# Optimization experiments

Hardware: AMD Instinct MI355X
Metric: run time of the kernel (lower is better)

Reference implementation:

```python
import jax, jax.numpy as jnp
import numpy as np

BASIS_SIZE = 256          # levels of the bitfield code
R_MAX = 1.0               # quantization range for normalized weights
QMAX = BASIS_SIZE // 2 - 1  # 127 -> symmetric int8-style grid
EPS = 1e-8


def setup_inputs() -> dict:
    key = jax.random.key(0)
    kx, kw, kb = jax.random.split(key, 3)
    B, S, D_IN, D_OUT = 4, 2048, 4096, 4096
    x = jax.random.normal(kx, (B, S, D_IN), dtype=jnp.float32)
    W = jax.random.normal(kw, (D_OUT, D_IN), dtype=jnp.float32)
    bias = jax.random.normal(kb, (D_OUT,), dtype=jnp.float32)
    return {"x": x, "W": W, "bias": bias}


def _bitfield_dequant_weight(W):
    # per-output-row L2 norm (p=2, dim=1 in torch)
    weight_norms = jnp.sqrt(jnp.sum(W * W, axis=1))          # [out]
    W_normalized = W / (weight_norms[:, None] + EPS)          # rows ~unit norm
    # bitfield encode/decode: uniform symmetric quantization to BASIS_SIZE
    # levels in [-R_MAX, R_MAX]
    scale = R_MAX / QMAX
    Wq = jnp.round(jnp.clip(W_normalized, -R_MAX, R_MAX) / scale) * scale
    return Wq, weight_norms


def reference(x, W, bias):
    Wq, weight_norms = _bitfield_dequant_weight(W)
    B, S, D_IN = x.shape
    x2 = x.reshape(-1, D_IN)                                  # [B*S, in]
    # bitfield matmul on normalized weights
    out_norm = jnp.einsum('nd,od->no', x2, Wq)                # [B*S, out]
    # denormalize (restore row norms) + bias epilogue
    out = out_norm * weight_norms
    out = out.reshape(B, S, -1) + bias
    return out
```

## Files before the change

### kernel.cpp

```cpp
#include <hip/hip_runtime.h>
#include <hip/hip_bf16.h>

typedef __attribute__((ext_vector_type(4))) int i32x4;
typedef __attribute__((address_space(3))) char lds3;

#define D_IN  4096
#define D_OUT 4096
#define M_TOT 8192
#define RSTRIDE ((size_t)64 * D_IN)

__device__ __forceinline__ void async16(const void* g, lds3* l) {
  __builtin_amdgcn_global_load_lds(
      (__attribute__((address_space(1))) void*)g,
      (__attribute__((address_space(3))) void*)l,
      16, 0, 0);
}

#define DSR(dst, addr, off) \
  asm volatile("ds_read_b128 %0, %1 offset:%2" : "=v"(dst) : "v"(addr), "i"(off))

__device__ __forceinline__ int pack4(float a, float b, float c, float d, float s) {
  int q0 = (int)rintf(a * s) & 255;
  int q1 = (int)rintf(b * s) & 255;
  int q2 = (int)rintf(c * s) & 255;
  int q3 = (int)rintf(d * s) & 255;
  return q0 | (q1 << 8) | (q2 << 16) | (q3 << 24);
}

__global__ void quant_x_kernel(const float* __restrict__ x, int* __restrict__ xq,
                               float* __restrict__ sx) {
  const int row = blockIdx.x * 4 + (threadIdx.x >> 6);
  const int lane = threadIdx.x & 63;
  const float4* xr = (const float4*)(x + (size_t)row * D_IN);

  float4 v[16];
  float mx = 0.f;
#pragma unroll
  for (int j = 0; j < 16; j++) {
    v[j] = xr[j * 64 + lane];
    mx = fmaxf(mx, fmaxf(fmaxf(fabsf(v[j].x), fabsf(v[j].y)),
                         fmaxf(fabsf(v[j].z), fabsf(v[j].w))));
  }
#pragma unroll
  for (int off = 32; off; off >>= 1) mx = fmaxf(mx, __shfl_xor(mx, off));
  if (lane == 0) sx[row] = mx * (1.0f / 127.0f);

  const float inv = 127.0f / mx;
  int* xqr = xq + (size_t)row * (D_IN / 4);
#pragma unroll
  for (int j = 0; j < 16; j++)
    xqr[j * 64 + lane] = pack4(v[j].x, v[j].y, v[j].z, v[j].w, inv);
}

__global__ void quant_w_kernel(const float* __restrict__ W, int* __restrict__ wq,
                               float* __restrict__ sn) {
  const int row = blockIdx.x * 4 + (threadIdx.x >> 6);
  const int lane = threadIdx.x & 63;
  const float4* wr = (const float4*)(W + (size_t)row * D_IN);

  float4 v[16];
  double ss = 0.0;
#pragma unroll
  for (int j = 0; j < 16; j++) {
    v[j] = wr[j * 64 + lane];
    ss += (double)v[j].x * v[j].x + (double)v[j].y * v[j].y +
          (double)v[j].z * v[j].z + (double)v[j].w * v[j].w;
  }
#pragma unroll
  for (int off = 32; off; off >>= 1) ss += __shfl_xor(ss, off);
  const float nrm = (float)sqrt(ss);
  if (lane == 0) sn[row] = nrm * (1.0f / 127.0f);

  const float den = nrm + 1e-8f;
  int* wqr = wq + (size_t)row * (D_IN / 4);
#pragma unroll
  for (int j = 0; j < 16; j++) {
    float e[4] = {v[j].x, v[j].y, v[j].z, v[j].w};
    int q[4];
#pragma unroll
    for (int c = 0; c < 4; c++) {
      float wn = e[c] / den;
      wn = fminf(1.0f, fmaxf(-1.0f, wn));
      q[c] = (int)rintf(wn * 127.0f) & 255;
    }
    wqr[j * 64 + lane] = q[0] | (q[1] << 8) | (q[2] << 16) | (q[3] << 24);
  }
}

template<int S, int VM, bool ISSUE, bool MF>
__device__ __forceinline__ void k_pipe(unsigned aA, unsigned aB,
                                       const char*& pA, const char*& pB,
                                       lds3* lA0, lds3* lB0,
                                       i32x4 (&fill)[8], i32x4 (&use)[8],
                                       i32x4 (&acc)[4][4]) {
  asm volatile("s_waitcnt vmcnt(%0)" :: "i"(VM));
  asm volatile("s_barrier" ::: "memory");
  if (ISSUE) {
    constexpr int T = ((S + 2) % 3) * 16384;
    async16(pA, lA0 + T);  async16(pA + RSTRIDE, lA0 + T + 4096);
    async16(pB, lB0 + T);  async16(pB + RSTRIDE, lB0 + T + 4096);
    pA += 64; pB += 64;
  }
  DSR(fill[0], aA, S * 16384 + 0);
  DSR(fill[1], aA, S * 16384 + 1024);
  DSR(fill[2], aA, S * 16384 + 2048);
  DSR(fill[3], aA, S * 16384 + 3072);
  DSR(fill[4], aB, S * 16384 + 8192 + 0);
  DSR(fill[5], aB, S * 16384 + 8192 + 1024);
  DSR(fill[6], aB, S * 16384 + 8192 + 2048);
  DSR(fill[7], aB, S * 16384 + 8192 + 3072);
  __builtin_amdgcn_sched_barrier(0);
  if (MF) {
    __builtin_amdgcn_s_setprio(1);
#pragma unroll
    for (int mi = 0; mi < 4; mi++)
#pragma unroll
      for (int ni = 0; ni < 4; ni++)
        acc[mi][ni] = __builtin_amdgcn_mfma_i32_16x16x64_i8(use[mi], use[4 + ni],
                                                            acc[mi][ni], 0, 0, 0);
    __builtin_amdgcn_s_setprio(0);
  }
  __builtin_amdgcn_sched_barrier(0);
  asm volatile("s_waitcnt lgkmcnt(0)"
               : "+v"(fill[0]), "+v"(fill[1]), "+v"(fill[2]), "+v"(fill[3]),
                 "+v"(fill[4]), "+v"(fill[5]), "+v"(fill[6]), "+v"(fill[7]));
}

__global__ __launch_bounds__(256, 3)
void gemm_i8_kernel(const char* __restrict__ A, const char* __restrict__ B,
                    const float* __restrict__ sx, const float* __restrict__ sn,
                    const float* __restrict__ bias, float* __restrict__ C) {
  __shared__ __align__(16) char smem[3 * 16384];

  const int t = threadIdx.x;
  const int lane = t & 63;
  const int wave = t >> 6;
  const int wm = wave >> 1, wn = wave & 1;
  const int m0 = blockIdx.y * 128;
  const int n0 = blockIdx.x * 128;

  const int srow = t >> 2;
  const int q = ((t & 3) - ((srow & 15) >> 1)) & 3;
  const char* gA = A + (size_t)(m0 + srow) * D_IN + q * 16;
  const char* gB = B + (size_t)(n0 + srow) * D_IN + q * 16;

  lds3* l3 = (lds3*)smem;
  lds3* lA0 = l3 + t * 16;
  lds3* lB0 = l3 + 8192 + t * 16;

  const int ml = lane & 15;
  const int g = lane >> 4;
  const unsigned cperm = (unsigned)((g + (ml >> 1)) & 3);
  const unsigned lds_base = (unsigned)(size_t)l3;
  const unsigned aA = lds_base + (wm * 64 + ml) * 64 + cperm * 16;
  const unsigned aB = lds_base + (wn * 64 + ml) * 64 + cperm * 16;

  i32x4 acc[4][4];
#pragma unroll
  for (int i = 0; i < 4; i++)
#pragma unroll
    for (int j = 0; j < 4; j++) acc[i][j] = (i32x4)0;

  i32x4 fA[8], fB[8];

  async16(gA, lA0);            async16(gA + RSTRIDE, lA0 + 4096);
  async16(gB, lB0);            async16(gB + RSTRIDE, lB0 + 4096);
  async16(gA + 64, lA0 + 16384);           async16(gA + 64 + RSTRIDE, lA0 + 16384 + 4096);
  async16(gB + 64, lB0 + 16384);           async16(gB + 64 + RSTRIDE, lB0 + 16384 + 4096);

  const char* pA = gA + 128;
  const char* pB = gB + 128;

  k_pipe<0, 4, true, false>(aA, aB, pA, pB, lA0, lB0, fA, fB, acc);
  k_pipe<1, 4, true, true >(aA, aB, pA, pB, lA0, lB0, fB, fA, acc);
  k_pipe<2, 4, true, true >(aA, aB, pA, pB, lA0, lB0, fA, fB, acc);
  k_pipe<0, 4, true, true >(aA, aB, pA, pB, lA0, lB0, fB, fA, acc);
  k_pipe<1, 4, true, true >(aA, aB, pA, pB, lA0, lB0, fA, fB, acc);
  k_pipe<2, 4, true, true >(aA, aB, pA, pB, lA0, lB0, fB, fA, acc);

#pragma unroll 1
  for (int tr = 0; tr < 9; ++tr) {
    k_pipe<0, 4, true, true>(aA, aB, pA, pB, lA0, lB0, fA, fB, acc);
    k_pipe<1, 4, true, true>(aA, aB, pA, pB, lA0, lB0, fB, fA, acc);
    k_pipe<2, 4, true, true>(aA, aB, pA, pB, lA0, lB0, fA, fB, acc);
    k_pipe<0, 4, true, true>(aA, aB, pA, pB, lA0, lB0, fB, fA, acc);
    k_pipe<1, 4, true, true>(aA, aB, pA, pB, lA0, lB0, fA, fB, acc);
    k_pipe<2, 4, true, true>(aA, aB, pA, pB, lA0, lB0, fB, fA, acc);
  }
  k_pipe<0, 4, true,  true>(aA, aB, pA, pB, lA0, lB0, fA, fB, acc);
  k_pipe<1, 4, true,  true>(aA, aB, pA, pB, lA0, lB0, fB, fA, acc);
  k_pipe<2, 4, false, true>(aA, aB, pA, pB, lA0, lB0, fA, fB, acc);
  k_pipe<0, 0, false, true>(aA, aB, pA, pB, lA0, lB0, fB, fA, acc);
#pragma unroll
  for (int mi = 0; mi < 4; mi++)
#pragma unroll
    for (int ni = 0; ni < 4; ni++)
      acc[mi][ni] = __builtin_amdgcn_mfma_i32_16x16x64_i8(fB[mi], fB[4 + ni],
                                                          acc[mi][ni], 0, 0, 0);

  float scn[4], bsv[4];
#pragma unroll
  for (int ni = 0; ni < 4; ni++) {
    const int col = n0 + wn * 64 + ni * 16 + ml;
    scn[ni] = sn[col];
    bsv[ni] = bias[col];
  }
#pragma unroll
  for (int mi = 0; mi < 4; mi++) {
    const int rbase = m0 + wm * 64 + mi * 16 + g * 4;
    float sxv[4];
#pragma unroll
    for (int r = 0; r < 4; r++) sxv[r] = sx[rbase + r];
#pragma unroll
    for (int ni = 0; ni < 4; ni++) {
      const int col = n0 + wn * 64 + ni * 16 + ml;
#pragma unroll
      for (int r = 0; r < 4; r++)
        C[(size_t)(rbase + r) * D_OUT + col] =
            (float)acc[mi][ni][r] * (sxv[r] * scn[ni]) + bsv[ni];
    }
  }
}

extern "C" void kernel_launch(void* const* d_in, const int* in_sizes, int n_in,
                              void* d_out, int out_size, void* d_ws, size_t ws_size,
                              hipStream_t stream) {
  const float* x    = (const float*)d_in[0];
  const float* W    = (const float*)d_in[1];
  const float* bias = (const float*)d_in[2];
  float* out = (float*)d_out;

  char* ws = (char*)d_ws;
  char*  xq = ws;
  char*  wq = ws + (size_t)M_TOT * D_IN;
  float* sx = (float*)(wq + (size_t)D_OUT * D_IN);
  float* sn = sx + M_TOT;

  quant_x_kernel<<<M_TOT / 4, 256, 0, stream>>>(x, (int*)xq, sx);
  quant_w_kernel<<<D_OUT / 4, 256, 0, stream>>>(W, (int*)wq, sn);
  dim3 grid(D_OUT / 128, M_TOT / 128);
  gemm_i8_kernel<<<grid, 256, 0, stream>>>(xq, wq, sx, sn, bias, out);
}
```

Baseline: 426.0 us.

## Restructure int8 GEMM to 256x256 tiles with 32x32 MFMA and swizzled grid

The GEMM kernel moves from 128x128 tiles with 4 waves to 256x256 tiles with 8 waves and 128-byte K steps. It switches from 16x16x64 to 32x32x32 int8 MFMA, double-buffers 128KB of LDS with an XOR swizzle, and staggers the A and B loads across the sub-phases of each K tile. The launch becomes a 1D grid remapped by a block-index swizzle for L2 locality. The aim is higher arithmetic intensity per byte of LDS and global traffic, at the cost of occupancy (2 blocks/CU requested, one likely fits given the LDS size) and many extra barriers per K tile.

```diff
diff --git a/kernel.cpp b/kernel.cpp
--- a/kernel.cpp
+++ b/kernel.cpp
@@ -1,13 +1,12 @@
 #include <hip/hip_runtime.h>
-#include <hip/hip_bf16.h>
 
 typedef __attribute__((ext_vector_type(4))) int i32x4;
+typedef __attribute__((ext_vector_type(16))) int i32x16;
 typedef __attribute__((address_space(3))) char lds3;
 
 #define D_IN  4096
 #define D_OUT 4096
 #define M_TOT 8192
-#define RSTRIDE ((size_t)64 * D_IN)
 
 __device__ __forceinline__ void async16(const void* g, lds3* l) {
   __builtin_amdgcn_global_load_lds(
@@ -87,137 +86,193 @@
   }
 }
 
-template<int S, int VM, bool ISSUE, bool MF>
-__device__ __forceinline__ void k_pipe(unsigned aA, unsigned aB,
-                                       const char*& pA, const char*& pB,
-                                       lds3* lA0, lds3* lB0,
-                                       i32x4 (&fill)[8], i32x4 (&use)[8],
-                                       i32x4 (&acc)[4][4]) {
+template<int BUF, int VM, bool ISSA, bool ISSB>
+__device__ __forceinline__ void ktile(const unsigned (&aAk)[4], const unsigned (&aBk)[4],
+                                      const char* pA, const char* pB,
+                                      lds3* lA, lds3* lB,
+                                      i32x4 (&af)[2][4], i32x4 (&bf)[8],
+                                      i32x16 (&acc)[4][2]) {
+  constexpr int AB = BUF * 32768;
+  constexpr int OB = (BUF ^ 1) * 32768;
+
+  DSR(bf[0], aBk[0], AB + 0);
+  DSR(bf[1], aBk[1], AB + 0);
+  DSR(bf[2], aBk[2], AB + 0);
+  DSR(bf[3], aBk[3], AB + 0);
+  DSR(bf[4], aBk[0], AB + 4096);
+  DSR(bf[5], aBk[1], AB + 4096);
+  DSR(bf[6], aBk[2], AB + 4096);
+  DSR(bf[7], aBk[3], AB + 4096);
+  DSR(af[0][0], aAk[0], AB + 0);
+  DSR(af[0][1], aAk[1], AB + 0);
+  DSR(af[0][2], aAk[2], AB + 0);
+  DSR(af[0][3], aAk[3], AB + 0);
+  if (ISSA) { async16(pA, lA + OB);
+              async16(pA + (size_t)64 * D_IN, lA + OB + 8192); }
+  asm volatile("s_barrier" ::: "memory");
+  asm volatile("s_waitcnt lgkmcnt(0)"
+               : "+v"(af[0][0]), "+v"(af[0][1]), "+v"(af[0][2]), "+v"(af[0][3]),
+                 "+v"(bf[0]), "+v"(bf[1]), "+v"(bf[2]), "+v"(bf[3]),
+                 "+v"(bf[4]), "+v"(bf[5]), "+v"(bf[6]), "+v"(bf[7]));
+  __builtin_amdgcn_sched_barrier(0);
+  __builtin_amdgcn_s_setprio(1);
+#pragma unroll
+  for (int kk = 0; kk < 4; kk++) {
+    acc[0][0] = __builtin_amdgcn_mfma_i32_32x32x32_i8(af[0][kk], bf[kk],     acc[0][0], 0, 0, 0);
+    acc[0][1] = __builtin_amdgcn_mfma_i32_32x32x32_i8(af[0][kk], bf[4 + kk], acc[0][1], 0, 0, 0);
+  }
+  __builtin_amdgcn_s_setprio(0);
+  __builtin_amdgcn_sched_barrier(0);
+  asm volatile("s_barrier" ::: "memory");
+
+  DSR(af[1][0], aAk[0], AB + 4096);
+  DSR(af[1][1], aAk[1], AB + 4096);
+  DSR(af[1][2], aAk[2], AB + 4096);
+  DSR(af[1][3], aAk[3], AB + 4096);
+  if (ISSA) { async16(pA + (size_t)128 * D_IN, lA + OB + 16384);
+              async16(pA + (size_t)192 * D_IN, lA + OB + 24576); }
+  asm volatile("s_barrier" ::: "memory");
+  asm volatile("s_waitcnt lgkmcnt(0)"
+               : "+v"(af[1][0]), "+v"(af[1][1]), "+v"(af[1][2]), "+v"(af[1][3]));
+  __builtin_amdgcn_sched_barrier(0);
+  __builtin_amdgcn_s_setprio(1);
+#pragma unroll
+  for (int kk = 0; kk < 4; kk++) {
+    acc[1][0] = __builtin_amdgcn_mfma_i32_32x32x32_i8(af[1][kk], bf[kk],     acc[1][0], 0, 0, 0);
+    acc[1][1] = __builtin_amdgcn_mfma_i32_32x32x32_i8(af[1][kk], bf[4 + kk], acc[1][1], 0, 0, 0);
+  }
+  __builtin_amdgcn_s_setprio(0);
+  __builtin_amdgcn_sched_barrier(0);
+  asm volatile("s_barrier" ::: "memory");
+
+  DSR(af[0][0], aAk[0], AB + 8192);
+  DSR(af[0][1], aAk[1], AB + 8192);
+  DSR(af[0][2], aAk[2], AB + 8192);
+  DSR(af[0][3], aAk[3], AB + 8192);
+  if (ISSB) { async16(pB, lB + AB);
+              async16(pB + (size_t)64 * D_IN, lB + AB + 8192); }
+  asm volatile("s_barrier" ::: "memory");
+  asm volatile("s_waitcnt lgkmcnt(0)"
+               : "+v"(af[0][0]), "+v"(af[0][1]), "+v"(af[0][2]), "+v"(af[0][3]));
+  __builtin_amdgcn_sched_barrier(0);
+  __builtin_amdgcn_s_setprio(1);
+#pragma unroll
+  for (int kk = 0; kk < 4; kk++) {
+    acc[2][0] = __builtin_amdgcn_mfma_i32_32x32x32_i8(af[0][kk], bf[kk],     acc[2][0], 0, 0, 0);
+    acc[2][1] = __builtin_amdgcn_mfma_i32_32x32x32_i8(af[0][kk], bf[4 + kk], acc[2][1], 0, 0, 0);
+  }
+  __builtin_amdgcn_s_setprio(0);
+  __builtin_amdgcn_sched_barrier(0);
+  asm volatile("s_barrier" ::: "memory");
+
+  DSR(af[1][0], aAk[0], AB + 12288);
+  DSR(af[1][1], aAk[1], AB + 12288);
+  DSR(af[1][2], aAk[2], AB + 12288);
+  DSR(af[1][3], aAk[3], AB + 12288);
+  if (ISSB) { async16(pB + (size_t)128 * D_IN, lB + AB + 16384);
+              async16(pB + (size_t)192 * D_IN, lB + AB + 24576); }
+  asm volatile("s_barrier" ::: "memory");
+  asm volatile("s_waitcnt lgkmcnt(0)"
+               : "+v"(af[1][0]), "+v"(af[1][1]), "+v"(af[1][2]), "+v"(af[1][3]));
+  __builtin_amdgcn_sched_barrier(0);
+  __builtin_amdgcn_s_setprio(1);
+#pragma unroll
+  for (int kk = 0; kk < 4; kk++) {
+    acc[3][0] = __builtin_amdgcn_mfma_i32_32x32x32_i8(af[1][kk], bf[kk],     acc[3][0], 0, 0, 0);
+    acc[3][1] = __builtin_amdgcn_mfma_i32_32x32x32_i8(af[1][kk], bf[4 + kk], acc[3][1], 0, 0, 0);
+  }
+  __builtin_amdgcn_s_setprio(0);
+  __builtin_amdgcn_sched_barrier(0);
   asm volatile("s_waitcnt vmcnt(%0)" :: "i"(VM));
   asm volatile("s_barrier" ::: "memory");
-  if (ISSUE) {
-    constexpr int T = ((S + 2) % 3) * 16384;
-    async16(pA, lA0 + T);  async16(pA + RSTRIDE, lA0 + T + 4096);
-    async16(pB, lB0 + T);  async16(pB + RSTRIDE, lB0 + T + 4096);
-    pA += 64; pB += 64;
-  }
-  DSR(fill[0], aA, S * 16384 + 0);
-  DSR(fill[1], aA, S * 16384 + 1024);
-  DSR(fill[2], aA, S * 16384 + 2048);
-  DSR(fill[3], aA, S * 16384 + 3072);
-  DSR(fill[4], aB, S * 16384 + 8192 + 0);
-  DSR(fill[5], aB, S * 16384 + 8192 + 1024);
-  DSR(fill[6], aB, S * 16384 + 8192 + 2048);
-  DSR(fill[7], aB, S * 16384 + 8192 + 3072);
-  __builtin_amdgcn_sched_barrier(0);
-  if (MF) {
-    __builtin_amdgcn_s_setprio(1);
-#pragma unroll
-    for (int mi = 0; mi < 4; mi++)
-#pragma unroll
-      for (int ni = 0; ni < 4; ni++)
-        acc[mi][ni] = __builtin_amdgcn_mfma_i32_16x16x64_i8(use[mi], use[4 + ni],
-                                                            acc[mi][ni], 0, 0, 0);
-    __builtin_amdgcn_s_setprio(0);
-  }
-  __builtin_amdgcn_sched_barrier(0);
-  asm volatile("s_waitcnt lgkmcnt(0)"
-               : "+v"(fill[0]), "+v"(fill[1]), "+v"(fill[2]), "+v"(fill[3]),
-                 "+v"(fill[4]), "+v"(fill[5]), "+v"(fill[6]), "+v"(fill[7]));
-}
-
-__global__ __launch_bounds__(256, 3)
+}
+
+__global__ __launch_bounds__(512, 2)
 void gemm_i8_kernel(const char* __restrict__ A, const char* __restrict__ B,
                     const float* __restrict__ sx, const float* __restrict__ sn,
                     const float* __restrict__ bias, float* __restrict__ C) {
-  __shared__ __align__(16) char smem[3 * 16384];
+  __shared__ __align__(16) char smem[131072];
 
   const int t = threadIdx.x;
   const int lane = t & 63;
   const int wave = t >> 6;
-  const int wm = wave >> 1, wn = wave & 1;
-  const int m0 = blockIdx.y * 128;
-  const int n0 = blockIdx.x * 128;
-
-  const int srow = t >> 2;
-  const int q = ((t & 3) - ((srow & 15) >> 1)) & 3;
-  const char* gA = A + (size_t)(m0 + srow) * D_IN + q * 16;
-  const char* gB = B + (size_t)(n0 + srow) * D_IN + q * 16;
-
+  const int wm = wave >> 2, wn = wave & 3;
+
+  const int bid = blockIdx.x;
+  const int swz = ((bid & 7) << 6) | (bid >> 3);
+  const int m0 = (swz >> 4) * 256;
+  const int n0 = (swz & 15) * 256;
+
+  const int srow = t >> 3;
+  const int sch  = (t & 7) ^ (srow & 7);
+  const char* gA = A + (size_t)(m0 + srow) * D_IN + sch * 16;
+  const char* gB = B + (size_t)(n0 + srow) * D_IN + sch * 16;
   lds3* l3 = (lds3*)smem;
-  lds3* lA0 = l3 + t * 16;
-  lds3* lB0 = l3 + 8192 + t * 16;
-
-  const int ml = lane & 15;
-  const int g = lane >> 4;
-  const unsigned cperm = (unsigned)((g + (ml >> 1)) & 3);
-  const unsigned lds_base = (unsigned)(size_t)l3;
-  const unsigned aA = lds_base + (wm * 64 + ml) * 64 + cperm * 16;
-  const unsigned aB = lds_base + (wn * 64 + ml) * 64 + cperm * 16;
-
-  i32x4 acc[4][4];
+  lds3* lA = l3 + t * 16;
+  lds3* lB = l3 + 65536 + t * 16;
+
+  const int l31 = lane & 31;
+  const int hi  = lane >> 5;
+  const int e   = lane & 7;
+  const unsigned base = (unsigned)(size_t)l3;
+  unsigned aAk[4], aBk[4];
+#pragma unroll
+  for (int kk = 0; kk < 4; kk++) {
+    const unsigned sw = (unsigned)(((kk * 2 + hi) ^ e) << 4);
+    aAk[kk] = base + (wm * 128 + l31) * 128 + sw;
+    aBk[kk] = base + 65536 + (wn * 64 + l31) * 128 + sw;
+  }
+
+  i32x16 acc[4][2];
 #pragma unroll
   for (int i = 0; i < 4; i++)
 #pragma unroll
-    for (int j = 0; j < 4; j++) acc[i][j] = (i32x4)0;
-
-  i32x4 fA[8], fB[8];
-
-  async16(gA, lA0);            async16(gA + RSTRIDE, lA0 + 4096);
-  async16(gB, lB0);            async16(gB + RSTRIDE, lB0 + 4096);
-  async16(gA + 64, lA0 + 16384);           async16(gA + 64 + RSTRIDE, lA0 + 16384 + 4096);
-  async16(gB + 64, lB0 + 16384);           async16(gB + 64 + RSTRIDE, lB0 + 16384 + 4096);
+    for (int j = 0; j < 2; j++) acc[i][j] = (i32x16)0;
+  i32x4 af[2][4], bf[8];
+
+  async16(gB,                       lB);
+  async16(gB + (size_t)64  * D_IN,  lB + 8192);
+  async16(gB + (size_t)128 * D_IN,  lB + 16384);
+  async16(gB + (size_t)192 * D_IN,  lB + 24576);
+  async16(gA,                       lA);
+  async16(gA + (size_t)64  * D_IN,  lA + 8192);
+  async16(gA + (size_t)128 * D_IN,  lA + 16384);
+  async16(gA + (size_t)192 * D_IN,  lA + 24576);
+  async16(gB + 128,                      lB + 32768);
+  async16(gB + 128 + (size_t)64  * D_IN, lB + 32768 + 8192);
+  async16(gB + 128 + (size_t)128 * D_IN, lB + 32768 + 16384);
+  async16(gB + 128 + (size_t)192 * D_IN, lB + 32768 + 24576);
+  asm volatile("s_waitcnt vmcnt(4)");
+  asm volatile("s_barrier" ::: "memory");
 
   const char* pA = gA + 128;
-  const char* pB = gB + 128;
-
-  k_pipe<0, 4, true, false>(aA, aB, pA, pB, lA0, lB0, fA, fB, acc);
-  k_pipe<1, 4, true, true >(aA, aB, pA, pB, lA0, lB0, fB, fA, acc);
-  k_pipe<2, 4, true, true >(aA, aB, pA, pB, lA0, lB0, fA, fB, acc);
-  k_pipe<0, 4, true, true >(aA, aB, pA, pB, lA0, lB0, fB, fA, acc);
-  k_pipe<1, 4, true, true >(aA, aB, pA, pB, lA0, lB0, fA, fB, acc);
-  k_pipe<2, 4, true, true >(aA, aB, pA, pB, lA0, lB0, fB, fA, acc);
+  const char* pB = gB + 256;
 
 #pragma unroll 1
-  for (int tr = 0; tr < 9; ++tr) {
-    k_pipe<0, 4, true, true>(aA, aB, pA, pB, lA0, lB0, fA, fB, acc);
-    k_pipe<1, 4, true, true>(aA, aB, pA, pB, lA0, lB0, fB, fA, acc);
-    k_pipe<2, 4, true, true>(aA, aB, pA, pB, lA0, lB0, fA, fB, acc);
-    k_pipe<0, 4, true, true>(aA, aB, pA, pB, lA0, lB0, fB, fA, acc);
-    k_pipe<1, 4, true, true>(aA, aB, pA, pB, lA0, lB0, fA, fB, acc);
-    k_pipe<2, 4, true, true>(aA, aB, pA, pB, lA0, lB0, fB, fA, acc);
-  }
-  k_pipe<0, 4, true,  true>(aA, aB, pA, pB, lA0, lB0, fA, fB, acc);
-  k_pipe<1, 4, true,  true>(aA, aB, pA, pB, lA0, lB0, fB, fA, acc);
-  k_pipe<2, 4, false, true>(aA, aB, pA, pB, lA0, lB0, fA, fB, acc);
-  k_pipe<0, 0, false, true>(aA, aB, pA, pB, lA0, lB0, fB, fA, acc);
-#pragma unroll
-  for (int mi = 0; mi < 4; mi++)
-#pragma unroll
-    for (int ni = 0; ni < 4; ni++)
-      acc[mi][ni] = __builtin_amdgcn_mfma_i32_16x16x64_i8(fB[mi], fB[4 + ni],
-                                                          acc[mi][ni], 0, 0, 0);
-
-  float scn[4], bsv[4];
-#pragma unroll
-  for (int ni = 0; ni < 4; ni++) {
-    const int col = n0 + wn * 64 + ni * 16 + ml;
-    scn[ni] = sn[col];
-    bsv[ni] = bias[col];
-  }
+  for (int it = 0; it < 15; ++it) {
+    ktile<0, 4, true, true>(aAk, aBk, pA, pB, lA, lB, af, bf, acc); pA += 128; pB += 128;
+    ktile<1, 4, true, true>(aAk, aBk, pA, pB, lA, lB, af, bf, acc); pA += 128; pB += 128;
+  }
+  ktile<0, 0, true,  false>(aAk, aBk, pA, pB, lA, lB, af, bf, acc); pA += 128;
+  ktile<1, 0, false, false>(aAk, aBk, pA, pB, lA, lB, af, bf, acc);
+
 #pragma unroll
   for (int mi = 0; mi < 4; mi++) {
-    const int rbase = m0 + wm * 64 + mi * 16 + g * 4;
-    float sxv[4];
-#pragma unroll
-    for (int r = 0; r < 4; r++) sxv[r] = sx[rbase + r];
-#pragma unroll
-    for (int ni = 0; ni < 4; ni++) {
-      const int col = n0 + wn * 64 + ni * 16 + ml;
-#pragma unroll
-      for (int r = 0; r < 4; r++)
-        C[(size_t)(rbase + r) * D_OUT + col] =
-            (float)acc[mi][ni][r] * (sxv[r] * scn[ni]) + bsv[ni];
+    const int rb = m0 + wm * 128 + mi * 32 + hi * 4;
+    float sxv[16];
+#pragma unroll
+    for (int r = 0; r < 16; r++) sxv[r] = sx[rb + (r & 3) + 8 * (r >> 2)];
+#pragma unroll
+    for (int ni = 0; ni < 2; ni++) {
+      const int col = n0 + wn * 64 + ni * 32 + l31;
+      const float scn = sn[col];
+      const float bv  = bias[col];
+#pragma unroll
+      for (int r = 0; r < 16; r++) {
+        const int row = rb + (r & 3) + 8 * (r >> 2);
+        C[(size_t)row * D_OUT + col] =
+            (float)acc[mi][ni][r] * (sxv[r] * scn) + bv;
+      }
     }
   }
 }
@@ -238,6 +293,5 @@
 
   quant_x_kernel<<<M_TOT / 4, 256, 0, stream>>>(x, (int*)xq, sx);
   quant_w_kernel<<<D_OUT / 4, 256, 0, stream>>>(W, (int*)wq, sn);
-  dim3 grid(D_OUT / 128, M_TOT / 128);
-  gemm_i8_kernel<<<grid, 256, 0, stream>>>(xq, wq, sx, sn, bias, out);
-}
+  gemm_i8_kernel<<<512, 512, 0, stream>>>(xq, wq, sx, sn, bias, out);
+}
```

Result: faster. 399.5 us (-6.2%).
